# Performance work log

Measured on AMD Instinct MI355X. Metric: run time of the kernel, lower is better.

## Reference

```python
import jax, jax.numpy as jnp
import numpy as np

S, B, D, H = 2048, 2, 1024, 16
DK = D // H
E, F = 8, 4096


def layernorm(x, g, b, eps=1e-5):
    mu = x.mean(-1, keepdims=True)
    var = x.var(-1, keepdims=True)
    return (x - mu) / jnp.sqrt(var + eps) * g + b


def setup_inputs() -> dict:
    key = jax.random.key(0)
    ks = jax.random.split(key, 10)
    s = 0.02
    rn = lambda k, shape: jax.random.normal(k, shape, jnp.float32) * s
    return dict(
        x=jax.random.normal(ks[0], (S, B, D), jnp.float32),
        ln1_g=jnp.ones((D,), jnp.float32), ln1_b=jnp.zeros((D,), jnp.float32),
        ln2_g=jnp.ones((D,), jnp.float32), ln2_b=jnp.zeros((D,), jnp.float32),
        wq=rn(ks[1], (D, D)), bq=jnp.zeros((D,), jnp.float32),
        wk=rn(ks[2], (D, D)), bk=jnp.zeros((D,), jnp.float32),
        wv=rn(ks[3], (D, D)), bv=jnp.zeros((D,), jnp.float32),
        wo=rn(ks[4], (D, D)), bo=jnp.zeros((D,), jnp.float32),
        w_gate=rn(ks[5], (D, E)), b_gate=jnp.zeros((E,), jnp.float32),
        w1=rn(ks[6], (E, D, F)), b1=jnp.zeros((E, F), jnp.float32),
        w2=rn(ks[7], (E, F, D)), b2=jnp.zeros((E, D), jnp.float32),
        mask=jnp.ones((S, S, B), jnp.bool_),
    )


def reference(x, ln1_g, ln1_b, ln2_g, ln2_b, wq, bq, wk, bk, wv, bv, wo, bo,
              w_gate, b_gate, w1, b1, w2, b2, mask):
    scale = 1.0 / np.sqrt(DK).astype(np.float32)
    # --- self attention (pre-norm) ---
    z = layernorm(x, ln1_g, ln1_b)
    q = (z @ wq + bq).reshape(S, B, H, DK)
    k = (z @ wk + bk).reshape(S, B, H, DK)
    v = (z @ wv + bv).reshape(S, B, H, DK)
    scores = jnp.einsum('sbhd,tbhd->stbh', q, k) * scale  # [Sq,Sk,B,H]
    scores = jnp.where(mask[:, :, :, None], scores, -jnp.inf)
    attn = jax.nn.softmax(scores, axis=1)  # softmax over key axis (dim=1)
    o = jnp.einsum('stbh,tbhd->sbhd', attn, v).reshape(S, B, D)
    x = x + (o @ wo + bo)
    # --- switch (top-1) MoE FFN (pre-norm) ---
    z = layernorm(x, ln2_g, ln2_b)
    flat = z.reshape(-1, D)  # [T, D], T = S*B
    probs = jax.nn.softmax(flat @ w_gate + b_gate, axis=-1)  # [T, E]
    pmax = probs.max(-1)
    routes = probs.argmax(-1)
    onehot = jax.nn.one_hot(routes, E, dtype=flat.dtype)  # [T, E]
    # dense dispatch: compute every expert, combine with one-hot mask
    h = jax.nn.relu(jnp.einsum('td,edf->etf', flat, w1) + b1[:, None, :])
    y = jnp.einsum('etf,efd->etd', h, w2) + b2[:, None, :]
    ff = jnp.einsum('etd,te->td', y, onehot) * pmax[:, None]
    out = x + ff.reshape(S, B, D)
    counts = onehot.sum(0)  # tokens per expert
    route_prob_sum = probs.sum(0)
    n_dropped = jnp.array(0, jnp.int32)  # drop_tokens=False
    return out, counts, route_prob_sum, n_dropped, pmax
```

## Files before the change

kernel.cpp:

```cpp
#include <hip/hip_runtime.h>

#define S_LEN 2048
#define B_SZ 2
#define D_DIM 1024
#define H_HEADS 16
#define DK_DIM 64
#define E_EXP 8
#define F_DIM 4096
#define T_TOK 4096

typedef unsigned short ush;
typedef __bf16 bf16x8 __attribute__((ext_vector_type(8)));
typedef float f32x4 __attribute__((ext_vector_type(4)));

__device__ __forceinline__ ush f2bf(float f) {
  union { __bf16 h; ush u; } cv;
  cv.h = (__bf16)f;
  return cv.u;
}

__device__ __forceinline__ float bf2f(ush u) {
  union { unsigned int i; float f; } cv;
  cv.i = ((unsigned int)u) << 16;
  return cv.f;
}

__device__ __forceinline__ void split2(float v, ush& h, ush& l) {
  ush hh = f2bf(v);
  h = hh;
  l = f2bf(v - bf2f(hh));
}

__device__ __forceinline__ void gload16(const void* g, void* l) {
  __builtin_amdgcn_global_load_lds(
      (const __attribute__((address_space(1))) unsigned int*)g,
      (__attribute__((address_space(3))) unsigned int*)l, 16, 0, 0);
}

#define MFMA(a, b, c) __builtin_amdgcn_mfma_f32_16x16x32_bf16(a, b, c, 0, 0, 0)

__global__ __launch_bounds__(256) void ln1_split(const float* __restrict__ x,
    const float* __restrict__ g, const float* __restrict__ b,
    ush* __restrict__ zh, ush* __restrict__ zl) {
  int t = blockIdx.x;
  float4 v = ((const float4*)(x + (size_t)t * D_DIM))[threadIdx.x];
  float s = v.x + v.y + v.z + v.w;
  float s2 = v.x * v.x + v.y * v.y + v.z * v.z + v.w * v.w;
#pragma unroll
  for (int off = 32; off > 0; off >>= 1) {
    s += __shfl_down(s, off);
    s2 += __shfl_down(s2, off);
  }
  __shared__ float red[8];
  int wid = threadIdx.x >> 6;
  if ((threadIdx.x & 63) == 0) { red[wid] = s; red[4 + wid] = s2; }
  __syncthreads();
  float sum = red[0] + red[1] + red[2] + red[3];
  float sq = red[4] + red[5] + red[6] + red[7];
  float mu = sum * (1.0f / D_DIM);
  float var = sq * (1.0f / D_DIM) - mu * mu;
  float rstd = rsqrtf(var + 1e-5f);
  float4 gg = ((const float4*)g)[threadIdx.x];
  float4 bb = ((const float4*)b)[threadIdx.x];
  float o[4];
  o[0] = (v.x - mu) * rstd * gg.x + bb.x;
  o[1] = (v.y - mu) * rstd * gg.y + bb.y;
  o[2] = (v.z - mu) * rstd * gg.z + bb.z;
  o[3] = (v.w - mu) * rstd * gg.w + bb.w;
  ushort4 uh, ul;
  split2(o[0], uh.x, ul.x); split2(o[1], uh.y, ul.y);
  split2(o[2], uh.z, ul.z); split2(o[3], uh.w, ul.w);
  *(ushort4*)(zh + (size_t)t * D_DIM + threadIdx.x * 4) = uh;
  *(ushort4*)(zl + (size_t)t * D_DIM + threadIdx.x * 4) = ul;
}

__global__ __launch_bounds__(256) void transpose_split(const float* __restrict__ in,
    ush* __restrict__ outh, ush* __restrict__ outl, int R, int C) {
  __shared__ float tile[32][33];
  int c0 = blockIdx.x * 32, r0 = blockIdx.y * 32;
  int tx = threadIdx.x & 31, ty = threadIdx.x >> 5;
#pragma unroll
  for (int i = 0; i < 4; i++)
    tile[ty + i * 8][tx] = in[(size_t)(r0 + ty + i * 8) * C + c0 + tx];
  __syncthreads();
#pragma unroll
  for (int i = 0; i < 4; i++) {
    float v = tile[tx][ty + i * 8];
    ush h, l;
    split2(v, h, l);
    size_t idx = (size_t)(c0 + ty + i * 8) * R + r0 + tx;
    outh[idx] = h;
    outl[idx] = l;
  }
}

__global__ __launch_bounds__(256) void transpose_bf16(const float* __restrict__ in,
    ush* __restrict__ out, int R, int C) {
  __shared__ float tile[32][33];
  int e = blockIdx.z;
  const float* ip = in + (size_t)e * R * C;
  ush* op = out + (size_t)e * R * C;
  int c0 = blockIdx.x * 32, r0 = blockIdx.y * 32;
  int tx = threadIdx.x & 31, ty = threadIdx.x >> 5;
#pragma unroll
  for (int i = 0; i < 4; i++)
    tile[ty + i * 8][tx] = ip[(size_t)(r0 + ty + i * 8) * C + c0 + tx];
  __syncthreads();
#pragma unroll
  for (int i = 0; i < 4; i++)
    op[(size_t)(c0 + ty + i * 8) * R + r0 + tx] = f2bf(tile[tx][ty + i * 8]);
}

__device__ __forceinline__ void split_gemm(const ush* __restrict__ Ah,
    const ush* __restrict__ Al, int lda, const ush* __restrict__ Bh,
    const ush* __restrict__ Bl, int ldb, int K, int tid, f32x4 acc[4][4],
    ush (*Ash)[64], ush (*Asl)[64], ush (*Bsh)[64], ush (*Bsl)[64]) {
  int lane = tid & 63, w = tid >> 6, quad = lane >> 4, ln15 = lane & 15;
  int srow = tid >> 3, scol = (tid & 7) * 8;
  int mb = (w >> 1) * 64, nb = (w & 1) * 64;
  for (int kb = 0; kb < K; kb += 64) {
    __syncthreads();
#pragma unroll
    for (int r = 0; r < 4; r++) {
      int rr = r * 32 + srow;
      gload16(Ah + (size_t)rr * lda + kb + scol, &Ash[rr][scol]);
      gload16(Al + (size_t)rr * lda + kb + scol, &Asl[rr][scol]);
      gload16(Bh + (size_t)rr * ldb + kb + scol, &Bsh[rr][scol]);
      gload16(Bl + (size_t)rr * ldb + kb + scol, &Bsl[rr][scol]);
    }
    __syncthreads();
#pragma unroll
    for (int kc = 0; kc < 2; kc++) {
      int kof = kc * 32 + quad * 8;
      bf16x8 avh[4], avl[4], bvh[4], bvl[4];
#pragma unroll
      for (int i = 0; i < 4; i++) {
        avh[i] = *(const bf16x8*)&Ash[mb + i * 16 + ln15][kof];
        avl[i] = *(const bf16x8*)&Asl[mb + i * 16 + ln15][kof];
        bvh[i] = *(const bf16x8*)&Bsh[nb + i * 16 + ln15][kof];
        bvl[i] = *(const bf16x8*)&Bsl[nb + i * 16 + ln15][kof];
      }
#pragma unroll
      for (int mi = 0; mi < 4; mi++)
#pragma unroll
        for (int ni = 0; ni < 4; ni++) {
          acc[mi][ni] = MFMA(avh[mi], bvh[ni], acc[mi][ni]);
          acc[mi][ni] = MFMA(avh[mi], bvl[ni], acc[mi][ni]);
          acc[mi][ni] = MFMA(avl[mi], bvh[ni], acc[mi][ni]);
        }
    }
  }
}

__global__ __launch_bounds__(256) void qkv_mfma(const ush* __restrict__ zh,
    const ush* __restrict__ zl, const ush* __restrict__ wT,
    const float* __restrict__ bq, const float* __restrict__ bk,
    const float* __restrict__ bv, ush* __restrict__ qh_, ush* __restrict__ kh_,
    ush* __restrict__ vth_) {
  __shared__ ush Ash[128][64], Asl[128][64], Bsh[128][64], Bsl[128][64];
  int z = blockIdx.z;
  int m0 = blockIdx.x * 128, n0 = blockIdx.y * 128;
  const ush* Bh = wT + (size_t)z * 2097152;
  const ush* Bl = Bh + 1048576;
  const float* bias = (z == 0) ? bq : (z == 1) ? bk : bv;
  ush* outh = (z == 0) ? qh_ : (z == 1) ? kh_ : vth_;
  int tid = threadIdx.x, lane = tid & 63, w = tid >> 6;
  int quad = lane >> 4, ln15 = lane & 15;
  int mb = (w >> 1) * 64, nb = (w & 1) * 64;
  f32x4 acc[4][4] = {};
  split_gemm(zh + (size_t)m0 * D_DIM, zl + (size_t)m0 * D_DIM, D_DIM,
             Bh + (size_t)n0 * D_DIM, Bl + (size_t)n0 * D_DIM, D_DIM, D_DIM,
             tid, acc, Ash, Asl, Bsh, Bsl);
#pragma unroll
  for (int mi = 0; mi < 4; mi++)
#pragma unroll
    for (int reg = 0; reg < 4; reg++) {
      int m = m0 + mb + mi * 16 + quad * 4 + reg;
      int s = m >> 1, b = m & 1;
#pragma unroll
      for (int ni = 0; ni < 4; ni++) {
        int n = n0 + nb + ni * 16 + ln15;
        float val = acc[mi][ni][reg] + bias[n];
        ush hh, ll;
        split2(val, hh, ll);
        int h = n >> 6, dk = n & 63;
        size_t idx;
        if (z < 2) idx = ((size_t)(b * H_HEADS + h) * S_LEN + s) * DK_DIM + dk;
        else       idx = ((size_t)(b * H_HEADS + h) * DK_DIM + dk) * S_LEN + s;
        outh[idx] = hh;
        outh[idx + 4194304] = ll;
      }
    }
}

__global__ __launch_bounds__(256, 2) void attn_mfma(const ush* __restrict__ qh,
    const ush* __restrict__ ql, const ush* __restrict__ kh,
    const ush* __restrict__ kl, const ush* __restrict__ vth,
    const ush* __restrict__ vtl, ush* __restrict__ oh, ush* __restrict__ ol) {
  int bh = blockIdx.y, q0 = blockIdx.x * 128;
  const size_t hoff = (size_t)bh * S_LEN * DK_DIM;
  __shared__ __align__(16) ush smem[32768];
  ush* Qh_ = smem;
  ush* Ql_ = smem + 8192;
  ush* Kh_ = smem + 16384;
  ush* Kl_ = smem + 20480;
  ush* Vh_ = smem + 24576;
  ush* Vl_ = smem + 28672;
  int tid = threadIdx.x, lane = tid & 63, w = tid >> 6;
  int quad = lane >> 4, ln15 = lane & 15;
  int srow = tid >> 3;
  int schunk = tid & 7;
  int gch = ((schunk ^ (srow & 7))) * 8;
  int sw = ln15 & 7;
#pragma unroll
  for (int p = 0; p < 4; p++) {
    int r = p * 32 + srow;
    gload16(qh + hoff + (size_t)(q0 + r) * DK_DIM + gch, Qh_ + r * 64 + schunk * 8);
    gload16(ql + hoff + (size_t)(q0 + r) * DK_DIM + gch, Ql_ + r * 64 + schunk * 8);
  }
  __syncthreads();
  bf16x8 Qf[2][2][2];
#pragma unroll
  for (int mi = 0; mi < 2; mi++)
#pragma unroll
    for (int kc = 0; kc < 2; kc++) {
      int row = w * 32 + mi * 16 + ln15;
      int ch = ((kc * 4 + quad) ^ sw) * 8;
      Qf[mi][kc][0] = *(const bf16x8*)(Qh_ + row * 64 + ch);
      Qf[mi][kc][1] = *(const bf16x8*)(Ql_ + row * 64 + ch);
    }
  const ush* pkh = kh + hoff + (size_t)srow * DK_DIM + schunk * 8;
  const ush* pkl = kl + hoff + (size_t)srow * DK_DIM + schunk * 8;
  const ush* pvh = vth + hoff + (size_t)srow * S_LEN + schunk * 8;
  const ush* pvl = vtl + hoff + (size_t)srow * S_LEN + schunk * 8;
  int ldst = srow * 64 + gch;
  float4 pk[2][2], pv[2][2];
#define LOAD_KV(KT) do {                                                       \
    size_t ko = (size_t)(KT) * (64 * DK_DIM);                                  \
    size_t vo = (size_t)(KT) * 64;                                             \
    _Pragma("unroll")                                                          \
    for (int p = 0; p < 2; p++) {                                              \
      pk[p][0] = *(const float4*)(pkh + ko + p * 32 * DK_DIM);                 \
      pk[p][1] = *(const float4*)(pkl + ko + p * 32 * DK_DIM);                 \
      pv[p][0] = *(const float4*)(pvh + vo + (size_t)p * 32 * S_LEN);          \
      pv[p][1] = *(const float4*)(pvl + vo + (size_t)p * 32 * S_LEN);          \
    }                                                                          \
  } while (0)
  LOAD_KV(0);
  f32x4 Oacc[2][4] = {};
  float m_i[2][4], l_i[2][4];
#pragma unroll
  for (int mi = 0; mi < 2; mi++)
#pragma unroll
    for (int r = 0; r < 4; r++) { m_i[mi][r] = -3e38f; l_i[mi][r] = 0.f; }
  const float cs = 0.18033688f;
  for (int kt = 0; kt < S_LEN / 64; kt++) {
    __syncthreads();
#pragma unroll
    for (int p = 0; p < 2; p++) {
      *(float4*)(Kh_ + p * 2048 + ldst) = pk[p][0];
      *(float4*)(Kl_ + p * 2048 + ldst) = pk[p][1];
      *(float4*)(Vh_ + p * 2048 + ldst) = pv[p][0];
      *(float4*)(Vl_ + p * 2048 + ldst) = pv[p][1];
    }
    __syncthreads();
    if (kt + 1 < S_LEN / 64) LOAD_KV(kt + 1);
    f32x4 S[2][4] = {};
#pragma unroll
    for (int kc = 0; kc < 2; kc++) {
      int ch = ((kc * 4 + quad) ^ sw) * 8;
      bf16x8 bkh[4], bkl[4];
#pragma unroll
      for (int ni = 0; ni < 4; ni++) {
        int row = ni * 16 + ln15;
        bkh[ni] = *(const bf16x8*)(Kh_ + row * 64 + ch);
        bkl[ni] = *(const bf16x8*)(Kl_ + row * 64 + ch);
      }
      __builtin_amdgcn_s_setprio(1);
#pragma unroll
      for (int mi = 0; mi < 2; mi++)
#pragma unroll
        for (int ni = 0; ni < 4; ni++) {
          S[mi][ni] = MFMA(Qf[mi][kc][0], bkh[ni], S[mi][ni]);
          S[mi][ni] = MFMA(Qf[mi][kc][0], bkl[ni], S[mi][ni]);
          S[mi][ni] = MFMA(Qf[mi][kc][1], bkh[ni], S[mi][ni]);
        }
      __builtin_amdgcn_s_setprio(0);
    }
    float mt[2][4];
#pragma unroll
    for (int mi = 0; mi < 2; mi++)
#pragma unroll
      for (int reg = 0; reg < 4; reg++)
        mt[mi][reg] = fmaxf(fmaxf(S[mi][0][reg], S[mi][1][reg]),
                            fmaxf(S[mi][2][reg], S[mi][3][reg]));
#pragma unroll
    for (int x = 1; x < 16; x <<= 1)
#pragma unroll
      for (int mi = 0; mi < 2; mi++)
#pragma unroll
        for (int reg = 0; reg < 4; reg++)
          mt[mi][reg] = fmaxf(mt[mi][reg], __shfl_xor(mt[mi][reg], x));
    float growth = -3e38f;
#pragma unroll
    for (int mi = 0; mi < 2; mi++)
#pragma unroll
      for (int reg = 0; reg < 4; reg++)
        growth = fmaxf(growth, mt[mi][reg] - m_i[mi][reg]);
    if (__any(growth > 44.3614195f)) {
#pragma unroll
      for (int mi = 0; mi < 2; mi++)
#pragma unroll
        for (int reg = 0; reg < 4; reg++) {
          float mnew = fmaxf(m_i[mi][reg], mt[mi][reg]);
          float a = __builtin_amdgcn_exp2f(cs * (m_i[mi][reg] - mnew));
          m_i[mi][reg] = mnew;
          l_i[mi][reg] *= a;
#pragma unroll
          for (int ni = 0; ni < 4; ni++) Oacc[mi][ni][reg] *= a;
        }
    }
    float ncm[2][4], ls[2][4] = {};
#pragma unroll
    for (int mi = 0; mi < 2; mi++)
#pragma unroll
      for (int reg = 0; reg < 4; reg++) ncm[mi][reg] = cs * m_i[mi][reg];
#pragma unroll
    for (int mi = 0; mi < 2; mi++)
#pragma unroll
      for (int ni = 0; ni < 4; ni++)
#pragma unroll
        for (int reg = 0; reg < 4; reg++) {
          float p = __builtin_amdgcn_exp2f(
              fmaf(S[mi][ni][reg], cs, -ncm[mi][reg]));
          ls[mi][reg] += p;
          ush hh, ll;
          split2(p, hh, ll);
          int row = w * 32 + mi * 16 + quad * 4 + reg;
          int cph = ((ni * 2 + (ln15 >> 3)) ^ ((quad * 4 + reg) & 7)) * 8 + (ln15 & 7);
          Qh_[row * 64 + cph] = hh;
          Ql_[row * 64 + cph] = ll;
        }
#pragma unroll
    for (int kc = 0; kc < 2; kc++) {
      int ch = ((kc * 4 + quad) ^ sw) * 8;
      bf16x8 aph[2], apl[2], bvh[4], bvl[4];
#pragma unroll
      for (int mi = 0; mi < 2; mi++) {
        int row = w * 32 + mi * 16 + ln15;
        aph[mi] = *(const bf16x8*)(Qh_ + row * 64 + ch);
        apl[mi] = *(const bf16x8*)(Ql_ + row * 64 + ch);
      }
#pragma unroll
      for (int ni = 0; ni < 4; ni++) {
        int row = ni * 16 + ln15;
        bvh[ni] = *(const bf16x8*)(Vh_ + row * 64 + ch);
        bvl[ni] = *(const bf16x8*)(Vl_ + row * 64 + ch);
      }
      __builtin_amdgcn_s_setprio(1);
#pragma unroll
      for (int mi = 0; mi < 2; mi++)
#pragma unroll
        for (int ni = 0; ni < 4; ni++) {
          Oacc[mi][ni] = MFMA(aph[mi], bvh[ni], Oacc[mi][ni]);
          Oacc[mi][ni] = MFMA(aph[mi], bvl[ni], Oacc[mi][ni]);
          Oacc[mi][ni] = MFMA(apl[mi], bvh[ni], Oacc[mi][ni]);
        }
      __builtin_amdgcn_s_setprio(0);
    }
#pragma unroll
    for (int x = 1; x < 16; x <<= 1)
#pragma unroll
      for (int mi = 0; mi < 2; mi++)
#pragma unroll
        for (int reg = 0; reg < 4; reg++)
          ls[mi][reg] += __shfl_xor(ls[mi][reg], x);
#pragma unroll
    for (int mi = 0; mi < 2; mi++)
#pragma unroll
      for (int reg = 0; reg < 4; reg++)
        l_i[mi][reg] += ls[mi][reg];
  }
#undef LOAD_KV
  float inv[2][4];
#pragma unroll
  for (int mi = 0; mi < 2; mi++)
#pragma unroll
    for (int reg = 0; reg < 4; reg++) inv[mi][reg] = 1.0f / l_i[mi][reg];
  int b = bh >> 4, h = bh & 15;
#pragma unroll
  for (int mi = 0; mi < 2; mi++)
#pragma unroll
    for (int ni = 0; ni < 4; ni++)
#pragma unroll
      for (int reg = 0; reg < 4; reg++) {
        float ov = Oacc[mi][ni][reg] * inv[mi][reg];
        int s = q0 + w * 32 + mi * 16 + quad * 4 + reg;
        int col = h * DK_DIM + ni * 16 + ln15;
        size_t idx = (size_t)(s * B_SZ + b) * D_DIM + col;
        ush hh, ll;
        split2(ov, hh, ll);
        oh[idx] = hh;
        ol[idx] = ll;
      }
}

__global__ __launch_bounds__(256) void wo_mfma(const ush* __restrict__ oh,
    const ush* __restrict__ ol, const ush* __restrict__ woTh,
    const float* __restrict__ bo, const float* __restrict__ x,
    float* __restrict__ out) {
  __shared__ ush Ash[128][64], Asl[128][64], Bsh[128][64], Bsl[128][64];
  int m0 = blockIdx.x * 128, n0 = blockIdx.y * 128;
  const ush* Bl = woTh + 1048576;
  int tid = threadIdx.x, lane = tid & 63, w = tid >> 6;
  int quad = lane >> 4, ln15 = lane & 15;
  int mb = (w >> 1) * 64, nb = (w & 1) * 64;
  f32x4 acc[4][4] = {};
  split_gemm(oh + (size_t)m0 * D_DIM, ol + (size_t)m0 * D_DIM, D_DIM,
             woTh + (size_t)n0 * D_DIM, Bl + (size_t)n0 * D_DIM, D_DIM, D_DIM,
             tid, acc, Ash, Asl, Bsh, Bsl);
#pragma unroll
  for (int mi = 0; mi < 4; mi++)
#pragma unroll
    for (int reg = 0; reg < 4; reg++) {
      int m = m0 + mb + mi * 16 + quad * 4 + reg;
#pragma unroll
      for (int ni = 0; ni < 4; ni++) {
        int n = n0 + nb + ni * 16 + ln15;
        size_t idx = (size_t)m * D_DIM + n;
        out[idx] = x[idx] + acc[mi][ni][reg] + bo[n];
      }
    }
}

__global__ __launch_bounds__(256) void moe1_mfma(const ush* __restrict__ zb,
    const ush* __restrict__ w1t, const float* __restrict__ b1,
    const int* __restrict__ list, const int* __restrict__ offs,
    ush* __restrict__ h) {
  int e = blockIdx.x;
  int n0 = blockIdx.y * 128;
  int mhalf = blockIdx.z;
  int off = offs[e], cnt = offs[e + 1] - off;
  __shared__ ush As[128][64], Bs[128][64];
  int tid = threadIdx.x, lane = tid & 63, w = tid >> 6;
  int colb = (lane & 7) * 8;
  int srw = w * 8 + (lane >> 3);
  const ush* gB[4];
  ush* lB[4];
#pragma unroll
  for (int r = 0; r < 4; r++) {
    int row = r * 32 + srw;
    gB[r] = w1t + ((size_t)e * F_DIM + n0 + row) * D_DIM + colb;
    lB[r] = &Bs[row][colb];
  }
  int mb = (w >> 1) * 64, nb = (w & 1) * 64;
  int quad = lane >> 4, ln15 = lane & 15;
  const float* be = b1 + (size_t)e * F_DIM;
  for (int m0 = mhalf * 128; m0 < cnt; m0 += 256) {
    const ush* gA[4];
    ush* lA[4];
#pragma unroll
    for (int r = 0; r < 4; r++) {
      int row = r * 32 + srw;
      int ra = m0 + row; if (ra > cnt - 1) ra = cnt - 1;
      int tok = list[off + ra];
      gA[r] = zb + (size_t)tok * D_DIM + colb;
      lA[r] = &As[row][colb];
    }
    f32x4 acc[4][4] = {};
    for (int kb = 0; kb < D_DIM; kb += 64) {
      __syncthreads();
#pragma unroll
      for (int r = 0; r < 4; r++) { gload16(gA[r] + kb, lA[r]); gload16(gB[r] + kb, lB[r]); }
      __syncthreads();
#pragma unroll
      for (int kc = 0; kc < 2; kc++) {
        int kof = kc * 32 + quad * 8;
        bf16x8 av[4], bv[4];
#pragma unroll
        for (int i = 0; i < 4; i++) {
          av[i] = *(const bf16x8*)&As[mb + i * 16 + ln15][kof];
          bv[i] = *(const bf16x8*)&Bs[nb + i * 16 + ln15][kof];
        }
#pragma unroll
        for (int mi = 0; mi < 4; mi++)
#pragma unroll
          for (int ni = 0; ni < 4; ni++)
            acc[mi][ni] = MFMA(av[mi], bv[ni], acc[mi][ni]);
      }
    }
#pragma unroll
    for (int mi = 0; mi < 4; mi++)
#pragma unroll
      for (int reg = 0; reg < 4; reg++) {
        int lm = m0 + mb + mi * 16 + quad * 4 + reg;
        if (lm < cnt) {
#pragma unroll
          for (int ni = 0; ni < 4; ni++) {
            int n = n0 + nb + ni * 16 + ln15;
            float v = acc[mi][ni][reg] + be[n];
            h[(size_t)(off + lm) * F_DIM + n] = f2bf(fmaxf(v, 0.f));
          }
        }
      }
  }
}

__global__ __launch_bounds__(256) void moe2_mfma(const ush* __restrict__ hb,
    const ush* __restrict__ w2t, const float* __restrict__ b2,
    const int* __restrict__ list, const int* __restrict__ offs,
    const float* __restrict__ pmax, float* __restrict__ out) {
  int e = blockIdx.x;
  int n0 = blockIdx.y * 128;
  int ks = blockIdx.z >> 1;
  int mhalf = blockIdx.z & 1;
  int off = offs[e], cnt = offs[e + 1] - off;
  size_t kbase = (size_t)ks * 1024;
  __shared__ ush As[128][64], Bs[128][64];
  int tid = threadIdx.x, lane = tid & 63, w = tid >> 6;
  int colb = (lane & 7) * 8;
  int srw = w * 8 + (lane >> 3);
  const ush* gB[4];
  ush* lB[4];
#pragma unroll
  for (int r = 0; r < 4; r++) {
    int row = r * 32 + srw;
    gB[r] = w2t + ((size_t)e * D_DIM + n0 + row) * F_DIM + kbase + colb;
    lB[r] = &Bs[row][colb];
  }
  int mb = (w >> 1) * 64, nb = (w & 1) * 64;
  int quad = lane >> 4, ln15 = lane & 15;
  const float* be = b2 + (size_t)e * D_DIM;
  for (int m0 = mhalf * 128; m0 < cnt; m0 += 256) {
    const ush* gA[4];
    ush* lA[4];
#pragma unroll
    for (int r = 0; r < 4; r++) {
      int row = r * 32 + srw;
      int ra = m0 + row; if (ra > cnt - 1) ra = cnt - 1;
      gA[r] = hb + (size_t)(off + ra) * F_DIM + kbase + colb;
      lA[r] = &As[row][colb];
    }
    f32x4 acc[4][4] = {};
    for (int kb = 0; kb < 1024; kb += 64) {
      __syncthreads();
#pragma unroll
      for (int r = 0; r < 4; r++) { gload16(gA[r] + kb, lA[r]); gload16(gB[r] + kb, lB[r]); }
      __syncthreads();
#pragma unroll
      for (int kc = 0; kc < 2; kc++) {
        int kof = kc * 32 + quad * 8;
        bf16x8 av[4], bv[4];
#pragma unroll
        for (int i = 0; i < 4; i++) {
          av[i] = *(const bf16x8*)&As[mb + i * 16 + ln15][kof];
          bv[i] = *(const bf16x8*)&Bs[nb + i * 16 + ln15][kof];
        }
#pragma unroll
        for (int mi = 0; mi < 4; mi++)
#pragma unroll
          for (int ni = 0; ni < 4; ni++)
            acc[mi][ni] = MFMA(av[mi], bv[ni], acc[mi][ni]);
      }
    }
#pragma unroll
    for (int mi = 0; mi < 4; mi++)
#pragma unroll
      for (int reg = 0; reg < 4; reg++) {
        int lm = m0 + mb + mi * 16 + quad * 4 + reg;
        if (lm < cnt) {
          int tok = list[off + lm];
          float p = pmax[tok];
#pragma unroll
          for (int ni = 0; ni < 4; ni++) {
            int n = n0 + nb + ni * 16 + ln15;
            float v = acc[mi][ni][reg];
            if (ks == 0) v += be[n];
            atomicAdd(&out[(size_t)tok * D_DIM + n], v * p);
          }
        }
      }
  }
}

__global__ __launch_bounds__(256) void ln2_gate(const float* __restrict__ x,
    const float* __restrict__ g, const float* __restrict__ b,
    const float* __restrict__ wg, const float* __restrict__ bg,
    ush* __restrict__ zb, float* __restrict__ pmax_out, int* __restrict__ route,
    float* __restrict__ rps_partial) {
  int t = blockIdx.x;
  float4 v = ((const float4*)(x + (size_t)t * D_DIM))[threadIdx.x];
  float s = v.x + v.y + v.z + v.w;
  float s2 = v.x * v.x + v.y * v.y + v.z * v.z + v.w * v.w;
#pragma unroll
  for (int off = 32; off > 0; off >>= 1) {
    s += __shfl_down(s, off);
    s2 += __shfl_down(s2, off);
  }
  __shared__ float red[8];
  int wid = threadIdx.x >> 6;
  if ((threadIdx.x & 63) == 0) { red[wid] = s; red[4 + wid] = s2; }
  __syncthreads();
  float sum = red[0] + red[1] + red[2] + red[3];
  float sq = red[4] + red[5] + red[6] + red[7];
  float mu = sum * (1.0f / D_DIM);
  float var = sq * (1.0f / D_DIM) - mu * mu;
  float rstd = rsqrtf(var + 1e-5f);
  float4 gg = ((const float4*)g)[threadIdx.x];
  float4 bb = ((const float4*)b)[threadIdx.x];
  float zz[4];
  zz[0] = (v.x - mu) * rstd * gg.x + bb.x;
  zz[1] = (v.y - mu) * rstd * gg.y + bb.y;
  zz[2] = (v.z - mu) * rstd * gg.z + bb.z;
  zz[3] = (v.w - mu) * rstd * gg.w + bb.w;
  ushort4 u;
  u.x = f2bf(zz[0]); u.y = f2bf(zz[1]); u.z = f2bf(zz[2]); u.w = f2bf(zz[3]);
  *(ushort4*)(zb + (size_t)t * D_DIM + threadIdx.x * 4) = u;
  int d0 = threadIdx.x * 4;
  float acc[8] = {};
  const float* w0 = wg + (size_t)d0 * E_EXP;
#pragma unroll
  for (int i = 0; i < 4; i++)
#pragma unroll
    for (int e = 0; e < 8; e++)
      acc[e] += zz[i] * w0[i * 8 + e];
#pragma unroll
  for (int off = 32; off > 0; off >>= 1)
#pragma unroll
    for (int e = 0; e < 8; e++) acc[e] += __shfl_down(acc[e], off);
  __shared__ float red2[4][8];
  if ((threadIdx.x & 63) == 0)
#pragma unroll
    for (int e = 0; e < 8; e++) red2[threadIdx.x >> 6][e] = acc[e];
  __syncthreads();
  if (threadIdx.x == 0) {
    float lg[8];
#pragma unroll
    for (int e = 0; e < 8; e++)
      lg[e] = red2[0][e] + red2[1][e] + red2[2][e] + red2[3][e] + bg[e];
    float mx = lg[0];
    int am = 0;
#pragma unroll
    for (int e = 1; e < 8; e++)
      if (lg[e] > mx) { mx = lg[e]; am = e; }
    float se = 0.f, pe[8];
#pragma unroll
    for (int e = 0; e < 8; e++) { pe[e] = expf(lg[e] - mx); se += pe[e]; }
    float inv = 1.0f / se;
    pmax_out[t] = inv;
    route[t] = am;
#pragma unroll
    for (int e = 0; e < 8; e++) rps_partial[(size_t)t * 8 + e] = pe[e] * inv;
  }
}

__global__ __launch_bounds__(256) void reduce_gate(const float* __restrict__ rps_partial,
    const int* __restrict__ route, float* __restrict__ rps, int* __restrict__ counts) {
  int e = blockIdx.x;
  float s = 0.f;
  int c = 0;
  for (int t = threadIdx.x; t < T_TOK; t += 256) {
    s += rps_partial[(size_t)t * 8 + e];
    c += (route[t] == e) ? 1 : 0;
  }
#pragma unroll
  for (int off = 32; off > 0; off >>= 1) {
    s += __shfl_down(s, off);
    c += __shfl_down(c, off);
  }
  __shared__ float sred[4];
  __shared__ int cred[4];
  int wid = threadIdx.x >> 6;
  if ((threadIdx.x & 63) == 0) { sred[wid] = s; cred[wid] = c; }
  __syncthreads();
  if (threadIdx.x == 0) {
    rps[e] = sred[0] + sred[1] + sred[2] + sred[3];
    counts[e] = cred[0] + cred[1] + cred[2] + cred[3];
  }
}

__global__ void init_kernel(int* cursor) {
  int i = threadIdx.x;
  if (i < E_EXP) cursor[i] = 0;
}

__global__ void offsets_kernel(const int* counts, int* offs, float* counts_f, float* ndrop) {
  if (threadIdx.x == 0) {
    int o = 0;
    for (int e = 0; e < E_EXP; e++) { offs[e] = o; o += counts[e]; }
    offs[E_EXP] = o;
    for (int e = 0; e < E_EXP; e++) counts_f[e] = (float)counts[e];
    *ndrop = 0.f;
  }
}

__global__ void scatter_kernel(const int* __restrict__ route, const int* __restrict__ offs,
                               int* __restrict__ cursor, int* __restrict__ list) {
  int t = blockIdx.x * 256 + threadIdx.x;
  int lane = threadIdx.x & 63;
  int e = (t < T_TOK) ? route[t] : -1;
#pragma unroll
  for (int ex = 0; ex < E_EXP; ex++) {
    unsigned long long mask = __ballot(e == ex);
    int cntw = __popcll(mask);
    if (cntw) {
      int leader = __ffsll((unsigned long long)mask) - 1;
      int base = 0;
      if (lane == leader) base = atomicAdd(&cursor[ex], cntw);
      base = __shfl(base, leader);
      if (e == ex) {
        int rank = __popcll(mask & ((1ull << lane) - 1));
        list[offs[ex] + base + rank] = t;
      }
    }
  }
}

extern "C" void kernel_launch(void* const* d_in, const int* in_sizes, int n_in,
                              void* d_out, int out_size, void* d_ws, size_t ws_size,
                              hipStream_t stream) {
  const float* x = (const float*)d_in[0];
  const float* ln1_g = (const float*)d_in[1];
  const float* ln1_b = (const float*)d_in[2];
  const float* ln2_g = (const float*)d_in[3];
  const float* ln2_b = (const float*)d_in[4];
  const float* wq = (const float*)d_in[5];
  const float* bq = (const float*)d_in[6];
  const float* wk = (const float*)d_in[7];
  const float* bk = (const float*)d_in[8];
  const float* wv = (const float*)d_in[9];
  const float* bv = (const float*)d_in[10];
  const float* wo = (const float*)d_in[11];
  const float* bo = (const float*)d_in[12];
  const float* wg = (const float*)d_in[13];
  const float* bg = (const float*)d_in[14];
  const float* w1 = (const float*)d_in[15];
  const float* b1 = (const float*)d_in[16];
  const float* w2 = (const float*)d_in[17];
  const float* b2 = (const float*)d_in[18];

  float* out = (float*)d_out;
  float* counts_f = out + (size_t)T_TOK * D_DIM;
  float* rps = counts_f + E_EXP;
  float* ndrop = rps + E_EXP;
  float* pmax = ndrop + 1;

  const size_t MB1 = 1048576;
  char* base = (char*)d_ws;
  ush* zh  = (ush*)(base + 0 * MB1);
  ush* zl  = (ush*)(base + 8 * MB1);
  ush* qh  = (ush*)(base + 16 * MB1);
  ush* ql  = (ush*)(base + 24 * MB1);
  ush* kh  = (ush*)(base + 32 * MB1);
  ush* kl  = (ush*)(base + 40 * MB1);
  ush* vth = (ush*)(base + 48 * MB1);
  ush* vtl = (ush*)(base + 56 * MB1);
  ush* wT  = (ush*)(base + 64 * MB1);
  ush* oh  = (ush*)(base + 80 * MB1);
  ush* ol  = (ush*)(base + 88 * MB1);
  ush* zb  = (ush*)(base + 64 * MB1);
  ush* hb  = (ush*)(base + 72 * MB1);
  int* route  = (int*)(base + 104 * MB1);
  int* list   = route + T_TOK;
  int* counts = list + T_TOK;
  int* offs   = counts + E_EXP;
  int* cursor = offs + E_EXP + 1;
  float* rps_partial = (float*)(base + 106 * MB1);
  ush* w1t = (ush*)(base + 0 * MB1);
  ush* w2t = (ush*)(base + 112 * MB1);

  ln1_split<<<T_TOK, 256, 0, stream>>>(x, ln1_g, ln1_b, zh, zl);
  dim3 gt(32, 32);
  transpose_split<<<gt, 256, 0, stream>>>(wq, wT + 0 * 2097152, wT + 0 * 2097152 + 1048576, D_DIM, D_DIM);
  transpose_split<<<gt, 256, 0, stream>>>(wk, wT + 1 * 2097152, wT + 1 * 2097152 + 1048576, D_DIM, D_DIM);
  transpose_split<<<gt, 256, 0, stream>>>(wv, wT + 2 * 2097152, wT + 2 * 2097152 + 1048576, D_DIM, D_DIM);
  transpose_split<<<gt, 256, 0, stream>>>(wo, wT + 3 * 2097152, wT + 3 * 2097152 + 1048576, D_DIM, D_DIM);
  dim3 gq(32, 8, 3);
  qkv_mfma<<<gq, 256, 0, stream>>>(zh, zl, wT, bq, bk, bv, qh, kh, vth);
  dim3 ga(S_LEN / 128, B_SZ * H_HEADS);
  attn_mfma<<<ga, 256, 0, stream>>>(qh, ql, kh, kl, vth, vtl, oh, ol);
  dim3 gt1(F_DIM / 32, D_DIM / 32, E_EXP);
  transpose_bf16<<<gt1, 256, 0, stream>>>(w1, w1t, D_DIM, F_DIM);
  dim3 gt2(D_DIM / 32, F_DIM / 32, E_EXP);
  transpose_bf16<<<gt2, 256, 0, stream>>>(w2, w2t, F_DIM, D_DIM);
  dim3 gw(32, 8);
  wo_mfma<<<gw, 256, 0, stream>>>(oh, ol, wT + 3 * 2097152, bo, x, out);
  init_kernel<<<1, 64, 0, stream>>>(cursor);
  ln2_gate<<<T_TOK, 256, 0, stream>>>(out, ln2_g, ln2_b, wg, bg, zb, pmax, route, rps_partial);
  reduce_gate<<<E_EXP, 256, 0, stream>>>(rps_partial, route, rps, counts);
  offsets_kernel<<<1, 64, 0, stream>>>(counts, offs, counts_f, ndrop);
  scatter_kernel<<<16, 256, 0, stream>>>(route, offs, cursor, list);
  dim3 gm1(E_EXP, F_DIM / 128, 2);
  moe1_mfma<<<gm1, 256, 0, stream>>>(zb, w1t, b1, list, offs, hb);
  dim3 gm2(E_EXP, D_DIM / 128, 8);
  moe2_mfma<<<gm2, 256, 0, stream>>>(hb, w2t, b2, list, offs, pmax, out);
}
```

Baseline: 984.4 us.

## Restructure attention loop with direct-to-LDS K/V loads, DPP reductions, bf16-only P

The attention kernel now keeps Q fragments loaded straight from global into registers and drops the Q tiles from shared memory. K and V tiles are streamed into LDS with global_load_lds, with V issued at the start of each tile and the next K prefetched after the softmax barrier, replacing the register-staged copies. Row max and sum reductions use DPP lane moves instead of shuffles. The probability matrix is kept only as a high bf16 part, with the row sum accumulated from the rounded values so normalisation stays consistent, cutting the PV MFMAs from three to two per tile. This reduces LDS footprint, VGPR pressure and MFMA count, at the cost of some precision in P and a tighter load/compute schedule that depends on barrier placement.

```diff
diff --git a/kernel.cpp b/kernel.cpp
--- a/kernel.cpp
+++ b/kernel.cpp
@@ -38,6 +38,27 @@
 }
 
 #define MFMA(a, b, c) __builtin_amdgcn_mfma_f32_16x16x32_bf16(a, b, c, 0, 0, 0)
+
+template <int CTRL>
+__device__ __forceinline__ float dpp_mov(float x) {
+  return __builtin_bit_cast(float,
+      __builtin_amdgcn_update_dpp(0, __builtin_bit_cast(int, x), CTRL, 0xF, 0xF,
+                                  true));
+}
+__device__ __forceinline__ float rmax16(float x) {
+  x = fmaxf(x, dpp_mov<0xB1>(x));
+  x = fmaxf(x, dpp_mov<0x4E>(x));
+  x = fmaxf(x, dpp_mov<0x141>(x));
+  x = fmaxf(x, dpp_mov<0x140>(x));
+  return x;
+}
+__device__ __forceinline__ float rsum16(float x) {
+  x += dpp_mov<0xB1>(x);
+  x += dpp_mov<0x4E>(x);
+  x += dpp_mov<0x141>(x);
+  x += dpp_mov<0x140>(x);
+  return x;
+}
 
 __global__ __launch_bounds__(256) void ln1_split(const float* __restrict__ x,
     const float* __restrict__ g, const float* __restrict__ b,
@@ -199,54 +220,34 @@
     const ush* __restrict__ vtl, ush* __restrict__ oh, ush* __restrict__ ol) {
   int bh = blockIdx.y, q0 = blockIdx.x * 128;
   const size_t hoff = (size_t)bh * S_LEN * DK_DIM;
-  __shared__ __align__(16) ush smem[32768];
-  ush* Qh_ = smem;
-  ush* Ql_ = smem + 8192;
-  ush* Kh_ = smem + 16384;
-  ush* Kl_ = smem + 20480;
-  ush* Vh_ = smem + 24576;
-  ush* Vl_ = smem + 28672;
+  __shared__ float4 smemv[3072];
+  ush* Ph_ = (ush*)smemv;
+  ush* Kh_ = (ush*)smemv + 8192;
+  ush* Kl_ = (ush*)smemv + 12288;
+  ush* Vh_ = (ush*)smemv + 16384;
+  ush* Vl_ = (ush*)smemv + 20480;
   int tid = threadIdx.x, lane = tid & 63, w = tid >> 6;
   int quad = lane >> 4, ln15 = lane & 15;
   int srow = tid >> 3;
   int schunk = tid & 7;
-  int gch = ((schunk ^ (srow & 7))) * 8;
+  int gch = (schunk ^ (srow & 7)) * 8;
   int sw = ln15 & 7;
 #pragma unroll
-  for (int p = 0; p < 4; p++) {
+  for (int p = 0; p < 2; p++) {
     int r = p * 32 + srow;
-    gload16(qh + hoff + (size_t)(q0 + r) * DK_DIM + gch, Qh_ + r * 64 + schunk * 8);
-    gload16(ql + hoff + (size_t)(q0 + r) * DK_DIM + gch, Ql_ + r * 64 + schunk * 8);
-  }
-  __syncthreads();
+    gload16(kh + hoff + (size_t)r * DK_DIM + gch, Kh_ + r * 64 + schunk * 8);
+    gload16(kl + hoff + (size_t)r * DK_DIM + gch, Kl_ + r * 64 + schunk * 8);
+  }
   bf16x8 Qf[2][2][2];
 #pragma unroll
   for (int mi = 0; mi < 2; mi++)
 #pragma unroll
     for (int kc = 0; kc < 2; kc++) {
-      int row = w * 32 + mi * 16 + ln15;
-      int ch = ((kc * 4 + quad) ^ sw) * 8;
-      Qf[mi][kc][0] = *(const bf16x8*)(Qh_ + row * 64 + ch);
-      Qf[mi][kc][1] = *(const bf16x8*)(Ql_ + row * 64 + ch);
-    }
-  const ush* pkh = kh + hoff + (size_t)srow * DK_DIM + schunk * 8;
-  const ush* pkl = kl + hoff + (size_t)srow * DK_DIM + schunk * 8;
-  const ush* pvh = vth + hoff + (size_t)srow * S_LEN + schunk * 8;
-  const ush* pvl = vtl + hoff + (size_t)srow * S_LEN + schunk * 8;
-  int ldst = srow * 64 + gch;
-  float4 pk[2][2], pv[2][2];
-#define LOAD_KV(KT) do {                                                       \
-    size_t ko = (size_t)(KT) * (64 * DK_DIM);                                  \
-    size_t vo = (size_t)(KT) * 64;                                             \
-    _Pragma("unroll")                                                          \
-    for (int p = 0; p < 2; p++) {                                              \
-      pk[p][0] = *(const float4*)(pkh + ko + p * 32 * DK_DIM);                 \
-      pk[p][1] = *(const float4*)(pkl + ko + p * 32 * DK_DIM);                 \
-      pv[p][0] = *(const float4*)(pvh + vo + (size_t)p * 32 * S_LEN);          \
-      pv[p][1] = *(const float4*)(pvl + vo + (size_t)p * 32 * S_LEN);          \
-    }                                                                          \
-  } while (0)
-  LOAD_KV(0);
+      size_t qidx = hoff + (size_t)(q0 + w * 32 + mi * 16 + ln15) * DK_DIM +
+                    (kc * 4 + quad) * 8;
+      Qf[mi][kc][0] = *(const bf16x8*)(qh + qidx);
+      Qf[mi][kc][1] = *(const bf16x8*)(ql + qidx);
+    }
   f32x4 Oacc[2][4] = {};
   float m_i[2][4], l_i[2][4];
 #pragma unroll
@@ -254,17 +255,16 @@
 #pragma unroll
     for (int r = 0; r < 4; r++) { m_i[mi][r] = -3e38f; l_i[mi][r] = 0.f; }
   const float cs = 0.18033688f;
+  __syncthreads();
   for (int kt = 0; kt < S_LEN / 64; kt++) {
-    __syncthreads();
 #pragma unroll
     for (int p = 0; p < 2; p++) {
-      *(float4*)(Kh_ + p * 2048 + ldst) = pk[p][0];
-      *(float4*)(Kl_ + p * 2048 + ldst) = pk[p][1];
-      *(float4*)(Vh_ + p * 2048 + ldst) = pv[p][0];
-      *(float4*)(Vl_ + p * 2048 + ldst) = pv[p][1];
-    }
-    __syncthreads();
-    if (kt + 1 < S_LEN / 64) LOAD_KV(kt + 1);
+      int r = p * 32 + srow;
+      gload16(vth + hoff + (size_t)r * S_LEN + kt * 64 + gch,
+              Vh_ + r * 64 + schunk * 8);
+      gload16(vtl + hoff + (size_t)r * S_LEN + kt * 64 + gch,
+              Vl_ + r * 64 + schunk * 8);
+    }
     f32x4 S[2][4] = {};
 #pragma unroll
     for (int kc = 0; kc < 2; kc++) {
@@ -291,16 +291,11 @@
 #pragma unroll
     for (int mi = 0; mi < 2; mi++)
 #pragma unroll
-      for (int reg = 0; reg < 4; reg++)
-        mt[mi][reg] = fmaxf(fmaxf(S[mi][0][reg], S[mi][1][reg]),
-                            fmaxf(S[mi][2][reg], S[mi][3][reg]));
-#pragma unroll
-    for (int x = 1; x < 16; x <<= 1)
-#pragma unroll
-      for (int mi = 0; mi < 2; mi++)
-#pragma unroll
-        for (int reg = 0; reg < 4; reg++)
-          mt[mi][reg] = fmaxf(mt[mi][reg], __shfl_xor(mt[mi][reg], x));
+      for (int reg = 0; reg < 4; reg++) {
+        float m = fmaxf(fmaxf(S[mi][0][reg], S[mi][1][reg]),
+                        fmaxf(S[mi][2][reg], S[mi][3][reg]));
+        mt[mi][reg] = rmax16(m);
+      }
     float growth = -3e38f;
 #pragma unroll
     for (int mi = 0; mi < 2; mi++)
@@ -333,23 +328,36 @@
         for (int reg = 0; reg < 4; reg++) {
           float p = __builtin_amdgcn_exp2f(
               fmaf(S[mi][ni][reg], cs, -ncm[mi][reg]));
-          ls[mi][reg] += p;
-          ush hh, ll;
-          split2(p, hh, ll);
+          ush hh = f2bf(p);
+          ls[mi][reg] += bf2f(hh);
           int row = w * 32 + mi * 16 + quad * 4 + reg;
           int cph = ((ni * 2 + (ln15 >> 3)) ^ ((quad * 4 + reg) & 7)) * 8 + (ln15 & 7);
-          Qh_[row * 64 + cph] = hh;
-          Ql_[row * 64 + cph] = ll;
-        }
+          Ph_[row * 64 + cph] = hh;
+        }
+#pragma unroll
+    for (int mi = 0; mi < 2; mi++)
+#pragma unroll
+      for (int reg = 0; reg < 4; reg++)
+        l_i[mi][reg] += rsum16(ls[mi][reg]);
+    __syncthreads();
+    if (kt + 1 < S_LEN / 64) {
+#pragma unroll
+      for (int p = 0; p < 2; p++) {
+        int r = p * 32 + srow;
+        gload16(kh + hoff + (size_t)((kt + 1) * 64 + r) * DK_DIM + gch,
+                Kh_ + r * 64 + schunk * 8);
+        gload16(kl + hoff + (size_t)((kt + 1) * 64 + r) * DK_DIM + gch,
+                Kl_ + r * 64 + schunk * 8);
+      }
+    }
 #pragma unroll
     for (int kc = 0; kc < 2; kc++) {
       int ch = ((kc * 4 + quad) ^ sw) * 8;
-      bf16x8 aph[2], apl[2], bvh[4], bvl[4];
+      bf16x8 ap[2], bvh[4], bvl[4];
 #pragma unroll
       for (int mi = 0; mi < 2; mi++) {
         int row = w * 32 + mi * 16 + ln15;
-        aph[mi] = *(const bf16x8*)(Qh_ + row * 64 + ch);
-        apl[mi] = *(const bf16x8*)(Ql_ + row * 64 + ch);
+        ap[mi] = *(const bf16x8*)(Ph_ + row * 64 + ch);
       }
 #pragma unroll
       for (int ni = 0; ni < 4; ni++) {
@@ -362,26 +370,13 @@
       for (int mi = 0; mi < 2; mi++)
 #pragma unroll
         for (int ni = 0; ni < 4; ni++) {
-          Oacc[mi][ni] = MFMA(aph[mi], bvh[ni], Oacc[mi][ni]);
-          Oacc[mi][ni] = MFMA(aph[mi], bvl[ni], Oacc[mi][ni]);
-          Oacc[mi][ni] = MFMA(apl[mi], bvh[ni], Oacc[mi][ni]);
+          Oacc[mi][ni] = MFMA(ap[mi], bvh[ni], Oacc[mi][ni]);
+          Oacc[mi][ni] = MFMA(ap[mi], bvl[ni], Oacc[mi][ni]);
         }
       __builtin_amdgcn_s_setprio(0);
     }
-#pragma unroll
-    for (int x = 1; x < 16; x <<= 1)
-#pragma unroll
-      for (int mi = 0; mi < 2; mi++)
-#pragma unroll
-        for (int reg = 0; reg < 4; reg++)
-          ls[mi][reg] += __shfl_xor(ls[mi][reg], x);
-#pragma unroll
-    for (int mi = 0; mi < 2; mi++)
-#pragma unroll
-      for (int reg = 0; reg < 4; reg++)
-        l_i[mi][reg] += ls[mi][reg];
-  }
-#undef LOAD_KV
+    __syncthreads();
+  }
   float inv[2][4];
 #pragma unroll
   for (int mi = 0; mi < 2; mi++)
```

After: 879.3 us. 10.7% less time.
